# Optimization experiments

Hardware: AMD Instinct MI355X
Metric: run time of the kernel (lower is better)

Reference implementation:

```python
import jax, jax.numpy as jnp
import numpy as np

N = 100000   # nodes
E = 1600000  # edges
IN, HID, CLS = 128, 64, 32


def gcn_conv(x, src, dst, W, b, num_nodes):
    """PyG-style GCNConv: out = D^{-1/2} (A+I) D^{-1/2} X W + b."""
    xw = x @ W  # transform first (matches PyG: propagate on transformed feats)
    loop = jnp.arange(num_nodes)
    src_f = jnp.concatenate([src, loop])
    dst_f = jnp.concatenate([dst, loop])
    ones = jnp.ones(src_f.shape[0], dtype=xw.dtype)
    deg = jax.ops.segment_sum(ones, dst_f, num_segments=num_nodes)
    dinv = jnp.where(deg > 0, jax.lax.rsqrt(deg), 0.0)
    norm = dinv[src_f] * dinv[dst_f]            # [E+N]
    msg = xw[src_f] * norm[:, None]             # gather + scale
    out = jax.ops.segment_sum(msg, dst_f, num_segments=num_nodes)
    return out + b


def setup_inputs() -> dict:
    key = jax.random.key(0)
    k = jax.random.split(key, 7)
    x = jax.random.normal(k[0], (N, IN), dtype=jnp.float32)
    edge_index = jax.random.randint(k[1], (2, E), 0, N)
    edge_attr = jax.random.normal(k[2], (E, 1), dtype=jnp.float32)
    W1 = jax.random.normal(k[3], (IN, HID), dtype=jnp.float32) / np.sqrt(IN)
    b1 = jnp.zeros((HID,), dtype=jnp.float32)
    W2 = jax.random.normal(k[4], (HID, CLS), dtype=jnp.float32) / np.sqrt(HID)
    b2 = jnp.zeros((CLS,), dtype=jnp.float32)
    return {"x": x, "edge_index": edge_index, "edge_attr": edge_attr,
            "W1": W1, "b1": b1, "W2": W2, "b2": b2}


def reference(x, edge_index, edge_attr, W1, b1, W2, b2):
    # edge_attr is unpacked by the original forward but unused by GCNConv
    src, dst = edge_index[0], edge_index[1]
    h = jax.nn.relu(gcn_conv(x, src, dst, W1, b1, N))
    return gcn_conv(h, src, dst, W2, b2, N)
```

## Files before the change

### kernel.cpp

```cpp
#include <hip/hip_runtime.h>
#include <hip/hip_fp16.h>

#define N_NODES 100000
#define N_EDGES 1600000
#define IN_F 128
#define HID_F 64
#define CLS_F 32

#define NBKT 512
#define BKT_NODES 196
#define NBLK 800
#define EPB 2000
#define CAPB_RAW 4096
#define CAPB 5120

typedef short s8v __attribute__((ext_vector_type(8)));
typedef float f4v __attribute__((ext_vector_type(4)));
typedef _Float16 h2v __attribute__((ext_vector_type(2)));

__device__ __forceinline__ unsigned short f2h(float f) {
    return __half_as_ushort(__float2half_rn(f));
}
__device__ __forceinline__ int packh2(float x, float y) {
    __half2 p = __floats2half2_rn(x, y);
    union { __half2 h; int i; } c; c.h = p; return c.i;
}

__device__ __forceinline__ void dot8(float* a, int4 v) {
#if __has_builtin(__builtin_amdgcn_fdot2)
    union { int4 i; h2v h[4]; } c; c.i = v;
    const h2v E0 = {(_Float16)1.f, (_Float16)0.f};
    const h2v E1 = {(_Float16)0.f, (_Float16)1.f};
#pragma unroll
    for (int j = 0; j < 4; j++) {
        a[2 * j]     = __builtin_amdgcn_fdot2(c.h[j], E0, a[2 * j], false);
        a[2 * j + 1] = __builtin_amdgcn_fdot2(c.h[j], E1, a[2 * j + 1], false);
    }
#else
    union { int4 i; __half2 h[4]; } c; c.i = v;
#pragma unroll
    for (int j = 0; j < 4; j++) {
        float2 f = __half22float2(c.h[j]);
        a[2 * j] += f.x; a[2 * j + 1] += f.y;
    }
#endif
}
__device__ __forceinline__ void dot4(float* a, int2 v) {
#if __has_builtin(__builtin_amdgcn_fdot2)
    union { int2 i; h2v h[2]; } c; c.i = v;
    const h2v E0 = {(_Float16)1.f, (_Float16)0.f};
    const h2v E1 = {(_Float16)0.f, (_Float16)1.f};
#pragma unroll
    for (int j = 0; j < 2; j++) {
        a[2 * j]     = __builtin_amdgcn_fdot2(c.h[j], E0, a[2 * j], false);
        a[2 * j + 1] = __builtin_amdgcn_fdot2(c.h[j], E1, a[2 * j + 1], false);
    }
#else
    union { int2 i; __half2 h[2]; } c; c.i = v;
#pragma unroll
    for (int j = 0; j < 2; j++) {
        float2 f = __half22float2(c.h[j]);
        a[2 * j] += f.x; a[2 * j + 1] += f.y;
    }
#endif
}


__global__ __launch_bounds__(256) void init_cursor_kernel(int* __restrict__ cursor) {
    int t = blockIdx.x * 256 + threadIdx.x;
    if (t < NBKT) cursor[t] = t * CAPB_RAW;
}

__global__ __launch_bounds__(256) void bucket_scatter_kernel(
        const int* __restrict__ src, const int* __restrict__ dst,
        int* __restrict__ cursor, unsigned* __restrict__ bkt) {
    __shared__ int h[NBKT];
    __shared__ int base[NBKT];
    __shared__ int lcur[NBKT];
    __shared__ unsigned pkS[EPB];
    __shared__ short gS[EPB];
    int t = threadIdx.x;
    for (int i = t; i < NBKT; i += 256) { h[i] = 0; lcur[i] = 0; }
    __syncthreads();

    int e0 = blockIdx.x * EPB;
    for (int i = t; i < EPB; i += 256) {
        int e = e0 + i;
        int d = dst[e];
        int g = d / BKT_NODES;
        pkS[i] = ((unsigned)(d - g * BKT_NODES) << 17) | (unsigned)src[e];
        gS[i] = (short)g;
        atomicAdd(&h[g], 1);
    }
    __syncthreads();

    for (int g = t; g < NBKT; g += 256)
        if (h[g] > 0) base[g] = atomicAdd(&cursor[g], h[g]);
    __syncthreads();

    for (int i = t; i < EPB; i += 256) {
        int g = gS[i];
        int p = base[g] + atomicAdd(&lcur[g], 1);
        bkt[p] = pkS[i];
    }
}

__global__ __launch_bounds__(256) void sort_bucket_kernel(const int* __restrict__ cursor,
                                                          const unsigned* __restrict__ bkt,
                                                          int* __restrict__ csr,
                                                          int* __restrict__ off,
                                                          int* __restrict__ endp,
                                                          float* __restrict__ dinv) {
    __shared__ int hist[BKT_NODES];
    __shared__ int loff[BKT_NODES];
    __shared__ int loffB[BKT_NODES];
    __shared__ int wt[4];
    __shared__ int csrS[CAPB];
    int b = blockIdx.x;
    int t = threadIdx.x;
    int s0 = b * CAPB_RAW;
    int nE = cursor[b] - s0;

    for (int i = t; i < BKT_NODES; i += 256) hist[i] = 0;
    __syncthreads();
    for (int i = t; i < nE; i += 256)
        atomicAdd(&hist[bkt[s0 + i] >> 17], 1);
    __syncthreads();

    int h0 = 0, h1 = 0;
    if (t < 98) { h0 = hist[2 * t]; h1 = hist[2 * t + 1]; }
    int p0 = (h0 + 7) & ~7;
    int p1 = (h1 + 7) & ~7;
    int sum = p0 + p1;
    int lane = t & 63, w = t >> 6;
    int s = sum;
#pragma unroll
    for (int d = 1; d < 64; d <<= 1) {
        int u = __shfl_up(s, d);
        if (lane >= d) s += u;
    }
    if (lane == 63) wt[w] = s;
    __syncthreads();
    int wbase = 0;
    for (int i = 0; i < w; i++) wbase += wt[i];
    int excl = wbase + s - sum;
    if (t < 98) {
        loff[2 * t] = excl;         loffB[2 * t] = excl;
        loff[2 * t + 1] = excl + p0; loffB[2 * t + 1] = excl + p0;
    }
    __syncthreads();

    for (int j = t; j < BKT_NODES; j += 256) {
        int n = b * BKT_NODES + j;
        if (n < N_NODES) {
            int c = hist[j];
            int o = b * CAPB + loff[j];
            off[n] = o;
            endp[n] = o + ((c + 7) & ~7);
            dinv[n] = rsqrtf((float)(c + 1));
        }
    }
    __syncthreads();

    for (int i = t; i < nE; i += 256) {
        unsigned pk = bkt[s0 + i];
        int dl = (int)(pk >> 17);
        int p = atomicAdd(&loff[dl], 1);
        csrS[p] = (int)(pk & 0x1FFFFu);
    }
    __syncthreads();

    for (int j = t; j < BKT_NODES; j += 256) {
        int c = hist[j];
        int bse = loffB[j];
        int pe = bse + ((c + 7) & ~7);
        for (int p = bse + c; p < pe; p++) csrS[p] = N_NODES;
    }
    __syncthreads();

    int padTot = wt[0] + wt[1] + wt[2] + wt[3];
    for (int i = t; i < padTot; i += 256) csr[b * CAPB + i] = csrS[i];
}

#define XBM 64
__global__ __launch_bounds__(256) void xw1_kernel(const float* __restrict__ x,
                                                  const float* __restrict__ W1,
                                                  const float* __restrict__ dinv,
                                                  unsigned short* __restrict__ y1h) {
    __shared__ __align__(16) unsigned short Wb[16 * 64 * 8];
    __shared__ __align__(16) unsigned short xb[XBM][IN_F + 8];

    int tid = threadIdx.x;

    for (int i = tid; i < IN_F * HID_F; i += 256) {
        int k = i >> 6, n = i & 63;
        int kc = k >> 5, kw = k & 31;
        int nt = n >> 4, nl = n & 15;
        int quad = kw >> 3, j = kw & 7;
        Wb[(((kc * 4 + nt) * 64) + quad * 16 + nl) * 8 + j] = f2h(W1[i]);
    }

    int nodeBase = blockIdx.x * XBM;
    {
        int snl = tid >> 2;
        int sk0 = (tid & 3) * 32;
        int n = nodeBase + snl;
#pragma unroll
        for (int kk = 0; kk < 32; kk += 4) {
            float4 v = make_float4(0.f, 0.f, 0.f, 0.f);
            if (n < N_NODES) v = *(const float4*)(x + (size_t)n * IN_F + sk0 + kk);
            ushort4 o;
            o.x = f2h(v.x); o.y = f2h(v.y); o.z = f2h(v.z); o.w = f2h(v.w);
            *(ushort4*)(&xb[snl][sk0 + kk]) = o;
        }
    }
    __syncthreads();

    int wave = tid >> 6, lane = tid & 63;
    int quad = lane >> 4, l15 = lane & 15;
    int rowBase = wave * 16;

    f4v acc[4];
#pragma unroll
    for (int i = 0; i < 4; i++) acc[i] = (f4v){0.f, 0.f, 0.f, 0.f};

#pragma unroll
    for (int kc = 0; kc < 4; kc++) {
        s8v a = *(const s8v*)(&xb[rowBase + l15][kc * 32 + quad * 8]);
#pragma unroll
        for (int nt = 0; nt < 4; nt++) {
            s8v b = *(const s8v*)(&Wb[((kc * 4 + nt) * 64 + lane) * 8]);
            acc[nt] = __builtin_amdgcn_mfma_f32_16x16x32_f16(a, b, acc[nt], 0, 0, 0);
        }
    }

    float dv[4];
    int n0 = nodeBase + rowBase + quad * 4;
#pragma unroll
    for (int r = 0; r < 4; r++)
        dv[r] = (n0 + r < N_NODES) ? dinv[n0 + r] : 0.f;
#pragma unroll
    for (int nt = 0; nt < 4; nt++) {
#pragma unroll
        for (int r = 0; r < 4; r++) {
            int n = n0 + r;
            if (n < N_NODES + 1)
                y1h[(size_t)n * HID_F + nt * 16 + l15] = f2h(acc[nt][r] * dv[r]);
        }
    }
}

__global__ __launch_bounds__(256) void gather1_kernel(
        const int* __restrict__ off, const int* __restrict__ endp,
        const int* __restrict__ csr, const unsigned short* __restrict__ y1h,
        const float* __restrict__ dinv, const float* __restrict__ b1,
        unsigned short* __restrict__ hout) {
    int tid = threadIdx.x;
    int wv = __builtin_amdgcn_readfirstlane(tid >> 6);
    int wave = blockIdx.x * 4 + wv;
    int nA = wave * 2, nB = nA + 1;
    int lane = tid & 63;
    int f = lane & 7;
    int g = lane >> 3;
    int fo = f * 16;

    int offA = off[nA], offB = off[nB];
    int lenA = endp[nA] - offA, lenB = endp[nB] - offB;
    int lmax = max(lenA, lenB);
    const int* pA = csr + offA + g;
    const int* pB = csr + offB + g;
    const char* yb = (const char*)y1h;

    float aA[8], aB[8];
#pragma unroll
    for (int j = 0; j < 8; j++) { aA[j] = 0.f; aB[j] = 0.f; }

    if (lmax > 0) {
        int rA = pA[0], rB = pB[0];
        int iA = (lenA > 0) ? rA : N_NODES;
        int iB = (lenB > 0) ? rB : N_NODES;
        int4 vA = *(const int4*)(yb + (size_t)iA * 128 + fo);
        int4 vB = *(const int4*)(yb + (size_t)iB * 128 + fo);
        int rA1 = pA[8], rB1 = pB[8];
        for (int t = 8; t < lmax; t += 8) {
            int inA = (t < lenA) ? rA1 : N_NODES;
            int inB = (t < lenB) ? rB1 : N_NODES;
            int4 nxA = *(const int4*)(yb + (size_t)inA * 128 + fo);
            int4 nxB = *(const int4*)(yb + (size_t)inB * 128 + fo);
            rA1 = pA[t + 8]; rB1 = pB[t + 8];
            dot8(aA, vA); dot8(aB, vB);
            vA = nxA; vB = nxB;
        }
        dot8(aA, vA); dot8(aB, vB);
    }

    float c8[8];
#pragma unroll
    for (int j = 0; j < 8; j++) {
        float sel = (lane < 32) ? aB[j] : aA[j];
        float oth = __shfl_xor(sel, 32);
        c8[j] = ((lane < 32) ? aA[j] : aB[j]) + oth;
    }
#pragma unroll
    for (int m = 8; m <= 16; m <<= 1)
#pragma unroll
        for (int j = 0; j < 8; j++) c8[j] += __shfl_xor(c8[j], m);

    int node = (lane < 32) ? nA : nB;

    int4 sv = *(const int4*)(yb + (size_t)node * 128 + fo);
    dot8(c8, sv);

    float dvA = dinv[nA], dvB = dinv[nB];
    float dvS = (lane < 32) ? dvA : dvB;
    float4 bl = *(const float4*)(b1 + 8 * f);
    float4 bh4 = *(const float4*)(b1 + 8 * f + 4);
    float bb[8] = {bl.x, bl.y, bl.z, bl.w, bh4.x, bh4.y, bh4.z, bh4.w};
    float h[8];
#pragma unroll
    for (int j = 0; j < 8; j++)
        h[j] = fmaxf(fmaf(c8[j], dvS, bb[j]), 0.f);
    int4 H;
    H.x = packh2(h[0], h[1]); H.y = packh2(h[2], h[3]);
    H.z = packh2(h[4], h[5]); H.w = packh2(h[6], h[7]);
    if ((lane & 31) < 8)
        *(int4*)((char*)hout + (size_t)node * 128 + fo) = H;
}

#define YBM 64
__global__ __launch_bounds__(256) void y2_kernel(const unsigned short* __restrict__ h,
                                                 const float* __restrict__ W2,
                                                 const float* __restrict__ dinv,
                                                 unsigned short* __restrict__ y2h) {
    __shared__ __align__(16) unsigned short Wb[2 * 2 * 64 * 8];
    __shared__ __align__(16) unsigned short hb[YBM][HID_F + 8];
    int tid = threadIdx.x;

    for (int i = tid; i < HID_F * CLS_F; i += 256) {
        int k = i >> 5, n = i & 31;
        int kc = k >> 5, kw = k & 31;
        int nt = n >> 4, nl = n & 15;
        int quad = kw >> 3, j = kw & 7;
        Wb[(((kc * 2 + nt) * 64) + quad * 16 + nl) * 8 + j] = f2h(W2[i]);
    }

    int nodeBase = blockIdx.x * YBM;
    {
        int row = tid >> 2, sseg = tid & 3;
        int n = nodeBase + row;
        int4 v0 = {0, 0, 0, 0}, v1 = {0, 0, 0, 0};
        if (n < N_NODES) {
            const char* hp = (const char*)h + (size_t)n * 128 + sseg * 32;
            v0 = *(const int4*)hp;
            v1 = *(const int4*)(hp + 16);
        }
        *(int4*)(&hb[row][sseg * 16]) = v0;
        *(int4*)(&hb[row][sseg * 16 + 8]) = v1;
    }
    __syncthreads();

    int wave = tid >> 6, lane = tid & 63;
    int quad = lane >> 4, l15 = lane & 15;
    int rowBase = wave * 16;

    f4v acc[2];
#pragma unroll
    for (int i = 0; i < 2; i++) acc[i] = (f4v){0.f, 0.f, 0.f, 0.f};

#pragma unroll
    for (int kc = 0; kc < 2; kc++) {
        s8v a = *(const s8v*)(&hb[rowBase + l15][kc * 32 + quad * 8]);
#pragma unroll
        for (int nt = 0; nt < 2; nt++) {
            s8v b = *(const s8v*)(&Wb[((kc * 2 + nt) * 64 + lane) * 8]);
            acc[nt] = __builtin_amdgcn_mfma_f32_16x16x32_f16(a, b, acc[nt], 0, 0, 0);
        }
    }

    float dv[4];
    int n0 = nodeBase + rowBase + quad * 4;
#pragma unroll
    for (int r = 0; r < 4; r++)
        dv[r] = (n0 + r < N_NODES) ? dinv[n0 + r] : 0.f;
#pragma unroll
    for (int nt = 0; nt < 2; nt++) {
#pragma unroll
        for (int r = 0; r < 4; r++) {
            int n = n0 + r;
            if (n < N_NODES + 1)
                y2h[(size_t)n * CLS_F + nt * 16 + l15] = f2h(acc[nt][r] * dv[r]);
        }
    }
}

__global__ __launch_bounds__(256) void gather2_kernel(const int* __restrict__ off,
                                                      const int* __restrict__ endp,
                                                      const int* __restrict__ csr,
                                                      const unsigned short* __restrict__ y2h,
                                                      const float* __restrict__ dinv,
                                                      const float* __restrict__ b2,
                                                      float* __restrict__ out) {
    int tid = threadIdx.x;
    int wv = __builtin_amdgcn_readfirstlane(tid >> 6);
    int wave = blockIdx.x * 4 + wv;
    int nA = wave * 2, nB = nA + 1;
    int lane = tid & 63;
    int f = lane & 7;
    int g = lane >> 3;
    int fo = f * 8;

    int offA = off[nA], offB = off[nB];
    int lenA = endp[nA] - offA, lenB = endp[nB] - offB;
    int lmax = max(lenA, lenB);
    const int* pA = csr + offA + g;
    const int* pB = csr + offB + g;
    const char* yb = (const char*)y2h;

    float aA[4], aB[4];
#pragma unroll
    for (int j = 0; j < 4; j++) { aA[j] = 0.f; aB[j] = 0.f; }

    if (lmax > 0) {
        int rA = pA[0], rB = pB[0];
        int iA = (lenA > 0) ? rA : N_NODES;
        int iB = (lenB > 0) ? rB : N_NODES;
        int2 vA = *(const int2*)(yb + (size_t)iA * 64 + fo);
        int2 vB = *(const int2*)(yb + (size_t)iB * 64 + fo);
        int rA1 = pA[8], rB1 = pB[8];
        for (int t = 8; t < lmax; t += 8) {
            int inA = (t < lenA) ? rA1 : N_NODES;
            int inB = (t < lenB) ? rB1 : N_NODES;
            int2 nxA = *(const int2*)(yb + (size_t)inA * 64 + fo);
            int2 nxB = *(const int2*)(yb + (size_t)inB * 64 + fo);
            rA1 = pA[t + 8]; rB1 = pB[t + 8];
            dot4(aA, vA); dot4(aB, vB);
            vA = nxA; vB = nxB;
        }
        dot4(aA, vA); dot4(aB, vB);
    }

    float c4[4];
#pragma unroll
    for (int j = 0; j < 4; j++) {
        float sel = (lane < 32) ? aB[j] : aA[j];
        float oth = __shfl_xor(sel, 32);
        c4[j] = ((lane < 32) ? aA[j] : aB[j]) + oth;
    }
#pragma unroll
    for (int m = 8; m <= 16; m <<= 1)
#pragma unroll
        for (int j = 0; j < 4; j++) c4[j] += __shfl_xor(c4[j], m);

    int node = (lane < 32) ? nA : nB;

    int2 sv = *(const int2*)(yb + (size_t)node * 64 + fo);
    dot4(c4, sv);

    float dvA = dinv[nA], dvB = dinv[nB];
    float dvS = (lane < 32) ? dvA : dvB;
    float4 b2v = *(const float4*)(b2 + 4 * f);
    float bbv[4] = {b2v.x, b2v.y, b2v.z, b2v.w};
    float4 o4;
    float* op = (float*)&o4;
#pragma unroll
    for (int j = 0; j < 4; j++)
        op[j] = fmaf(c4[j], dvS, bbv[j]);
    if ((lane & 31) < 8)
        *(float4*)(out + (size_t)node * CLS_F + f * 4) = o4;
}

extern "C" void kernel_launch(void* const* d_in, const int* in_sizes, int n_in,
                              void* d_out, int out_size, void* d_ws, size_t ws_size,
                              hipStream_t stream) {
    const float* x  = (const float*)d_in[0];
    const int*   ei = (const int*)d_in[1];
    const float* W1 = (const float*)d_in[3];
    const float* b1 = (const float*)d_in[4];
    const float* W2 = (const float*)d_in[5];
    const float* b2 = (const float*)d_in[6];
    float* out = (float*)d_out;

    const int* src = ei;
    const int* dst = ei + N_EDGES;

    char* ws = (char*)d_ws;
    size_t npad = ((size_t)N_NODES * 4 + 255) / 256 * 256;
    float* dinv = (float*)ws;
    int*   off  = (int*)(ws + npad);
    int*   endp = (int*)(ws + 2 * npad);
    int*   cursor = (int*)(ws + 3 * npad);
    int*   csr  = (int*)(ws + 3 * npad + 2048);
    char*  rbase = (char*)csr + (size_t)(NBKT + 1) * CAPB * 4;
    unsigned* bkt = (unsigned*)rbase;
    unsigned short* y1h = (unsigned short*)rbase;
    unsigned short* y2h = (unsigned short*)(rbase + (size_t)(N_NODES + 1) * HID_F * 2);
    unsigned short* hbuf = (unsigned short*)((char*)y2h + (size_t)(N_NODES + 1) * CLS_F * 2);

    dim3 blk(256);
    init_cursor_kernel  <<<dim3(2), blk, 0, stream>>>(cursor);
    bucket_scatter_kernel<<<dim3(NBLK), blk, 0, stream>>>(src, dst, cursor, bkt);
    sort_bucket_kernel  <<<dim3(NBKT), blk, 0, stream>>>(cursor, bkt, csr, off, endp, dinv);
    xw1_kernel          <<<dim3((N_NODES + XBM - 1) / XBM), blk, 0, stream>>>(x, W1, dinv, y1h);
    gather1_kernel      <<<dim3(N_NODES / 8), blk, 0, stream>>>(off, endp, csr, y1h, dinv, b1, hbuf);
    y2_kernel           <<<dim3((N_NODES + YBM) / YBM), blk, 0, stream>>>(hbuf, W2, dinv, y2h);
    gather2_kernel      <<<dim3(N_NODES / 8), blk, 0, stream>>>(off, endp, csr, y2h, dinv, b2, out);
}
```

Baseline: 221.9 us.

## Fuse bucket sort with XW1 GEMM and move dinv scaling into gather1

Merges the per-bucket CSR sort and the X·W1 MFMA transform into one launch, with block index choosing the role, so the two independent stages share the GPU and one launch is saved. To remove xw1's dependence on dinv, the source-side D^{-1/2} scaling moves into gather1: each gathered neighbour row is multiplied by its dinv through an fma instead of being summed directly. The cursor init kernel is replaced by a memset, with bucket bases added at use time. Gather1 now makes an extra per-edge dinv load and does fma work. Dinv gets padded to N+1 so the pad index is safe, and bkt no longer aliases y1h, which the concurrent blocks require.

Result: faster. 213.6 us (-3.8%).

```diff
diff --git a/kernel.cpp b/kernel.cpp
--- a/kernel.cpp
+++ b/kernel.cpp
@@ -13,6 +13,7 @@
 #define EPB 2000
 #define CAPB_RAW 4096
 #define CAPB 5120
+#define XW_BLOCKS 1563
 
 typedef short s8v __attribute__((ext_vector_type(8)));
 typedef float f4v __attribute__((ext_vector_type(4)));
@@ -26,25 +27,13 @@
     union { __half2 h; int i; } c; c.h = p; return c.i;
 }
 
-__device__ __forceinline__ void dot8(float* a, int4 v) {
-#if __has_builtin(__builtin_amdgcn_fdot2)
-    union { int4 i; h2v h[4]; } c; c.i = v;
-    const h2v E0 = {(_Float16)1.f, (_Float16)0.f};
-    const h2v E1 = {(_Float16)0.f, (_Float16)1.f};
-#pragma unroll
-    for (int j = 0; j < 4; j++) {
-        a[2 * j]     = __builtin_amdgcn_fdot2(c.h[j], E0, a[2 * j], false);
-        a[2 * j + 1] = __builtin_amdgcn_fdot2(c.h[j], E1, a[2 * j + 1], false);
-    }
-#else
-    union { int4 i; __half2 h[4]; } c; c.i = v;
-#pragma unroll
-    for (int j = 0; j < 4; j++) {
-        float2 f = __half22float2(c.h[j]);
-        a[2 * j] += f.x; a[2 * j + 1] += f.y;
-    }
-#endif
-}
+__device__ __forceinline__ void mix8(float* a, int4 v, float dv) {
+    union { int4 i; __half h[8]; } c; c.i = v;
+#pragma unroll
+    for (int j = 0; j < 8; j++)
+        a[j] = fmaf(__half2float(c.h[j]), dv, a[j]);
+}
+
 __device__ __forceinline__ void dot4(float* a, int2 v) {
 #if __has_builtin(__builtin_amdgcn_fdot2)
     union { int2 i; h2v h[2]; } c; c.i = v;
@@ -65,11 +54,6 @@
 #endif
 }
 
-
-__global__ __launch_bounds__(256) void init_cursor_kernel(int* __restrict__ cursor) {
-    int t = blockIdx.x * 256 + threadIdx.x;
-    if (t < NBKT) cursor[t] = t * CAPB_RAW;
-}
 
 __global__ __launch_bounds__(256) void bucket_scatter_kernel(
         const int* __restrict__ src, const int* __restrict__ dst,
@@ -95,7 +79,7 @@
     __syncthreads();
 
     for (int g = t; g < NBKT; g += 256)
-        if (h[g] > 0) base[g] = atomicAdd(&cursor[g], h[g]);
+        if (h[g] > 0) base[g] = g * CAPB_RAW + atomicAdd(&cursor[g], h[g]);
     __syncthreads();
 
     for (int i = t; i < EPB; i += 256) {
@@ -105,21 +89,21 @@
     }
 }
 
-__global__ __launch_bounds__(256) void sort_bucket_kernel(const int* __restrict__ cursor,
-                                                          const unsigned* __restrict__ bkt,
-                                                          int* __restrict__ csr,
-                                                          int* __restrict__ off,
-                                                          int* __restrict__ endp,
-                                                          float* __restrict__ dinv) {
-    __shared__ int hist[BKT_NODES];
-    __shared__ int loff[BKT_NODES];
-    __shared__ int loffB[BKT_NODES];
-    __shared__ int wt[4];
-    __shared__ int csrS[CAPB];
-    int b = blockIdx.x;
+#define XBM 64
+#define SMEM_BYTES 33792
+
+__device__ __forceinline__ void sort_body(char* smem, int b,
+        const int* __restrict__ cursor, const unsigned* __restrict__ bkt,
+        int* __restrict__ csr, int* __restrict__ off, int* __restrict__ endp,
+        float* __restrict__ dinv) {
+    int* hist  = (int*)smem;
+    int* loff  = hist + BKT_NODES;
+    int* loffB = loff + BKT_NODES;
+    int* wt    = loffB + BKT_NODES;
+    int* csrS  = wt + 4;
     int t = threadIdx.x;
     int s0 = b * CAPB_RAW;
-    int nE = cursor[b] - s0;
+    int nE = cursor[b];
 
     for (int i = t; i < BKT_NODES; i += 256) hist[i] = 0;
     __syncthreads();
@@ -182,14 +166,12 @@
     for (int i = t; i < padTot; i += 256) csr[b * CAPB + i] = csrS[i];
 }
 
-#define XBM 64
-__global__ __launch_bounds__(256) void xw1_kernel(const float* __restrict__ x,
-                                                  const float* __restrict__ W1,
-                                                  const float* __restrict__ dinv,
-                                                  unsigned short* __restrict__ y1h) {
-    __shared__ __align__(16) unsigned short Wb[16 * 64 * 8];
-    __shared__ __align__(16) unsigned short xb[XBM][IN_F + 8];
-
+__device__ __forceinline__ void xw1_body(char* smem, int xb_id,
+        const float* __restrict__ x, const float* __restrict__ W1,
+        unsigned short* __restrict__ y1h) {
+    unsigned short* Wb = (unsigned short*)smem;
+    unsigned short (*xbuf)[IN_F + 8] =
+        (unsigned short (*)[IN_F + 8])(smem + 16384);
     int tid = threadIdx.x;
 
     for (int i = tid; i < IN_F * HID_F; i += 256) {
@@ -200,7 +182,7 @@
         Wb[(((kc * 4 + nt) * 64) + quad * 16 + nl) * 8 + j] = f2h(W1[i]);
     }
 
-    int nodeBase = blockIdx.x * XBM;
+    int nodeBase = xb_id * XBM;
     {
         int snl = tid >> 2;
         int sk0 = (tid & 3) * 32;
@@ -211,7 +193,7 @@
             if (n < N_NODES) v = *(const float4*)(x + (size_t)n * IN_F + sk0 + kk);
             ushort4 o;
             o.x = f2h(v.x); o.y = f2h(v.y); o.z = f2h(v.z); o.w = f2h(v.w);
-            *(ushort4*)(&xb[snl][sk0 + kk]) = o;
+            *(ushort4*)(&xbuf[snl][sk0 + kk]) = o;
         }
     }
     __syncthreads();
@@ -226,7 +208,7 @@
 
 #pragma unroll
     for (int kc = 0; kc < 4; kc++) {
-        s8v a = *(const s8v*)(&xb[rowBase + l15][kc * 32 + quad * 8]);
+        s8v a = *(const s8v*)(&xbuf[rowBase + l15][kc * 32 + quad * 8]);
 #pragma unroll
         for (int nt = 0; nt < 4; nt++) {
             s8v b = *(const s8v*)(&Wb[((kc * 4 + nt) * 64 + lane) * 8]);
@@ -234,20 +216,29 @@
         }
     }
 
-    float dv[4];
     int n0 = nodeBase + rowBase + quad * 4;
-#pragma unroll
-    for (int r = 0; r < 4; r++)
-        dv[r] = (n0 + r < N_NODES) ? dinv[n0 + r] : 0.f;
 #pragma unroll
     for (int nt = 0; nt < 4; nt++) {
 #pragma unroll
         for (int r = 0; r < 4; r++) {
             int n = n0 + r;
             if (n < N_NODES + 1)
-                y1h[(size_t)n * HID_F + nt * 16 + l15] = f2h(acc[nt][r] * dv[r]);
-        }
-    }
+                y1h[(size_t)n * HID_F + nt * 16 + l15] = f2h(acc[nt][r]);
+        }
+    }
+}
+
+__global__ __launch_bounds__(256) void sort_xw1_kernel(
+        const int* __restrict__ cursor, const unsigned* __restrict__ bkt,
+        int* __restrict__ csr, int* __restrict__ off, int* __restrict__ endp,
+        float* __restrict__ dinv, const float* __restrict__ x,
+        const float* __restrict__ W1, unsigned short* __restrict__ y1h) {
+    __shared__ __align__(16) char smem[SMEM_BYTES];
+    int b = blockIdx.x;
+    if (b < NBKT)
+        sort_body(smem, b, cursor, bkt, csr, off, endp, dinv);
+    else
+        xw1_body(smem, b - NBKT, x, W1, y1h);
 }
 
 __global__ __launch_bounds__(256) void gather1_kernel(
@@ -279,19 +270,21 @@
         int rA = pA[0], rB = pB[0];
         int iA = (lenA > 0) ? rA : N_NODES;
         int iB = (lenB > 0) ? rB : N_NODES;
+        float dvA = dinv[iA], dvB = dinv[iB];
         int4 vA = *(const int4*)(yb + (size_t)iA * 128 + fo);
         int4 vB = *(const int4*)(yb + (size_t)iB * 128 + fo);
         int rA1 = pA[8], rB1 = pB[8];
         for (int t = 8; t < lmax; t += 8) {
             int inA = (t < lenA) ? rA1 : N_NODES;
             int inB = (t < lenB) ? rB1 : N_NODES;
+            float ndvA = dinv[inA], ndvB = dinv[inB];
             int4 nxA = *(const int4*)(yb + (size_t)inA * 128 + fo);
             int4 nxB = *(const int4*)(yb + (size_t)inB * 128 + fo);
             rA1 = pA[t + 8]; rB1 = pB[t + 8];
-            dot8(aA, vA); dot8(aB, vB);
-            vA = nxA; vB = nxB;
-        }
-        dot8(aA, vA); dot8(aB, vB);
+            mix8(aA, vA, dvA); mix8(aB, vB, dvB);
+            vA = nxA; vB = nxB; dvA = ndvA; dvB = ndvB;
+        }
+        mix8(aA, vA, dvA); mix8(aB, vB, dvB);
     }
 
     float c8[8];
@@ -307,12 +300,12 @@
         for (int j = 0; j < 8; j++) c8[j] += __shfl_xor(c8[j], m);
 
     int node = (lane < 32) ? nA : nB;
-
-    int4 sv = *(const int4*)(yb + (size_t)node * 128 + fo);
-    dot8(c8, sv);
-
     float dvA = dinv[nA], dvB = dinv[nB];
     float dvS = (lane < 32) ? dvA : dvB;
+
+    int4 sv = *(const int4*)(yb + (size_t)node * 128 + fo);
+    mix8(c8, sv, dvS);
+
     float4 bl = *(const float4*)(b1 + 8 * f);
     float4 bh4 = *(const float4*)(b1 + 8 * f + 4);
     float bb[8] = {bl.x, bl.y, bl.z, bl.w, bh4.x, bh4.y, bh4.z, bh4.w};
@@ -484,24 +477,27 @@
     const int* dst = ei + N_EDGES;
 
     char* ws = (char*)d_ws;
-    size_t npad = ((size_t)N_NODES * 4 + 255) / 256 * 256;
-    float* dinv = (float*)ws;
-    int*   off  = (int*)(ws + npad);
-    int*   endp = (int*)(ws + 2 * npad);
-    int*   cursor = (int*)(ws + 3 * npad);
-    int*   csr  = (int*)(ws + 3 * npad + 2048);
-    char*  rbase = (char*)csr + (size_t)(NBKT + 1) * CAPB * 4;
-    unsigned* bkt = (unsigned*)rbase;
-    unsigned short* y1h = (unsigned short*)rbase;
-    unsigned short* y2h = (unsigned short*)(rbase + (size_t)(N_NODES + 1) * HID_F * 2);
-    unsigned short* hbuf = (unsigned short*)((char*)y2h + (size_t)(N_NODES + 1) * CLS_F * 2);
+    size_t npad = ((size_t)(N_NODES + 1) * 4 + 255) / 256 * 256;
+    float* dinv   = (float*)ws;
+    int*   cursor = (int*)(ws + npad);
+    int*   off    = (int*)(ws + npad + 2048);
+    int*   endp   = (int*)(ws + 2 * npad + 2048);
+    int*   csr    = (int*)(ws + 3 * npad + 2048);
+    char*  p = (char*)csr + (size_t)(NBKT + 1) * CAPB * 4;
+    unsigned* bkt = (unsigned*)p;
+    p += (size_t)NBKT * CAPB_RAW * 4;
+    unsigned short* y1h = (unsigned short*)p;
+    p += (size_t)(N_NODES + 1) * HID_F * 2;
+    unsigned short* y2h = (unsigned short*)p;
+    p += (size_t)(N_NODES + 1) * CLS_F * 2;
+    unsigned short* hbuf = (unsigned short*)p;
 
     dim3 blk(256);
-    init_cursor_kernel  <<<dim3(2), blk, 0, stream>>>(cursor);
+    hipMemsetAsync(ws, 0, npad + 2048, stream);
     bucket_scatter_kernel<<<dim3(NBLK), blk, 0, stream>>>(src, dst, cursor, bkt);
-    sort_bucket_kernel  <<<dim3(NBKT), blk, 0, stream>>>(cursor, bkt, csr, off, endp, dinv);
-    xw1_kernel          <<<dim3((N_NODES + XBM - 1) / XBM), blk, 0, stream>>>(x, W1, dinv, y1h);
-    gather1_kernel      <<<dim3(N_NODES / 8), blk, 0, stream>>>(off, endp, csr, y1h, dinv, b1, hbuf);
-    y2_kernel           <<<dim3((N_NODES + YBM) / YBM), blk, 0, stream>>>(hbuf, W2, dinv, y2h);
-    gather2_kernel      <<<dim3(N_NODES / 8), blk, 0, stream>>>(off, endp, csr, y2h, dinv, b2, out);
-}
+    sort_xw1_kernel<<<dim3(NBKT + XW_BLOCKS), blk, 0, stream>>>(
+        cursor, bkt, csr, off, endp, dinv, x, W1, y1h);
+    gather1_kernel<<<dim3(N_NODES / 8), blk, 0, stream>>>(off, endp, csr, y1h, dinv, b1, hbuf);
+    y2_kernel<<<dim3((N_NODES + YBM) / YBM), blk, 0, stream>>>(hbuf, W2, dinv, y2h);
+    gather2_kernel<<<dim3(N_NODES / 8), blk, 0, stream>>>(off, endp, csr, y2h, dinv, b2, out);
+}
```
